# Kernel optimization log

Measured on AMD Instinct MI355X. Metric: run time of the kernel, lower is better.

## Reference

```python
import jax, jax.numpy as jnp
import numpy as np

NUM_BASE = 92
NUM_NOVEL = 40
GAMMA = 2.0
ALPHA = 0.25
DISTIL_FACTOR = 1.0
BSZ, N_DET, DIM_FEAT, DIM_HID, DIM_EMB = 16, 48, 2048, 1024, 512
EMB_HALF = DIM_EMB // 2


def _pair_ids(n):
    # all ordered pairs (i, j), i != j  (trajid2pairid)
    s, o = np.meshgrid(np.arange(n), np.arange(n), indexing='ij')
    m = s != o
    return s[m].astype(np.int32), o[m].astype(np.int32)


def _norm(x, eps=1e-12):
    # F.normalize(dim=-1)
    return x / jnp.maximum(jnp.linalg.norm(x, axis=-1, keepdims=True), eps)


def _sigmoid_focal_loss(logits, targets):
    # torchvision.ops.sigmoid_focal_loss, alpha=0.25, gamma=2, reduction='none'
    p = jax.nn.sigmoid(logits)
    ce = jnp.maximum(logits, 0) - logits * targets + jnp.log1p(jnp.exp(-jnp.abs(logits)))
    p_t = p * targets + (1.0 - p) * (1.0 - targets)
    loss = ce * (1.0 - p_t) ** GAMMA
    a_t = ALPHA * targets + (1.0 - ALPHA) * (1.0 - targets)
    return a_t * loss


def setup_inputs() -> dict:
    key = jax.random.key(0)
    ks = jax.random.split(key, 12)
    sids_np, oids_np = _pair_ids(N_DET)
    P = sids_np.shape[0]  # 2256 pairs per video
    w = lambda k, shape, s=0.02: jax.random.normal(k, shape, dtype=jnp.float32) * s
    return {
        'det_feats': jax.random.normal(ks[0], (BSZ, N_DET, DIM_FEAT), dtype=jnp.float32),
        'traj_embds': jax.random.normal(ks[1], (BSZ, N_DET, EMB_HALF), dtype=jnp.float32),
        'relpos_feats': jax.random.normal(ks[2], (BSZ, P, 12), dtype=jnp.float32),
        'classifier_weights': _norm(jax.random.normal(ks[3], (NUM_BASE, DIM_EMB), dtype=jnp.float32)) / np.sqrt(2.0),
        'W1': w(ks[4], (2 * DIM_FEAT, DIM_HID)), 'b1': jnp.zeros((DIM_HID,), jnp.float32),
        'W2': w(ks[5], (DIM_HID, DIM_HID)), 'b2': jnp.zeros((DIM_HID,), jnp.float32),
        'W3': w(ks[6], (DIM_HID, DIM_EMB)),
        'R1': w(ks[7], (12, 256), 0.1), 'rb1': jnp.zeros((256,), jnp.float32),
        'R2': w(ks[8], (256, DIM_EMB), 0.1),
        'temperature': jnp.full((1,), 0.02, dtype=jnp.float32),
        'labels': jax.random.randint(ks[9], (BSZ, P, 1 + NUM_BASE + NUM_NOVEL), 0, 2, dtype=jnp.int32),
        'sids': jnp.asarray(sids_np),
        'oids': jnp.asarray(oids_np),
    }


def reference(det_feats, traj_embds, relpos_feats, classifier_weights,
              W1, b1, W2, b2, W3, R1, rb1, R2, temperature,
              labels, sids, oids):
    Df = det_feats.shape[-1]
    De = traj_embds.shape[-1]
    # gather subject / object features for all pairs, flatten batch
    s_f = det_feats[:, sids, :].reshape(-1, Df)   # [N, Df]
    o_f = det_feats[:, oids, :].reshape(-1, Df)
    so = jnp.concatenate([s_f, o_f], axis=-1)      # [N, 2*Df]
    # trajpair_proj MLP
    h = jax.nn.relu(so @ W1 + b1)
    h = jax.nn.relu(h @ W2 + b2)
    so_proj = h @ W3                                # [N, dim_emb]
    so_n = _norm(so_proj)
    # relpos branch
    rp = relpos_feats.reshape(-1, relpos_feats.shape[-1])
    re = jax.nn.relu(rp @ R1 + rb1) @ R2
    re = _norm(re)
    combined = _norm(so_n + re)
    logits = (combined @ classifier_weights.T) / temperature  # [N, num_base]
    # cls_loss_on_base
    lab = labels.reshape(-1, 1 + NUM_BASE + NUM_NOVEL).astype(logits.dtype)
    pos_mask = jnp.any(lab[:, 1:1 + NUM_BASE] > 0, axis=-1)
    neg_mask = lab[:, 0] > 0
    lab_base = lab[:, 1:1 + NUM_BASE]
    fl_pos = _sigmoid_focal_loss(logits, lab_base)
    pos_den = jnp.maximum(pos_mask.sum(), 1).astype(logits.dtype) * NUM_BASE
    pos_loss = jnp.sum(fl_pos * pos_mask[:, None]) / pos_den
    fl_neg = _sigmoid_focal_loss(logits, jnp.zeros_like(logits))
    neg_den = jnp.maximum(neg_mask.sum(), 1).astype(logits.dtype) * NUM_BASE
    neg_loss = jnp.sum(fl_neg * neg_mask[:, None]) / neg_den
    # distillation L1 loss
    s_e = traj_embds[:, sids, :].reshape(-1, De)
    o_e = traj_embds[:, oids, :].reshape(-1, De)
    distil_target = jnp.concatenate([s_e, o_e], axis=-1)  # [N, dim_emb]
    distil_loss = jnp.mean(jnp.abs(distil_target - so_proj)) * DISTIL_FACTOR
    total_loss = pos_loss + neg_loss + distil_loss
    return total_loss
```

## Files before the change

### kernel.cpp

```cpp
#include <hip/hip_runtime.h>
#include <math.h>

constexpr int BSZ   = 16;
constexpr int NDET  = 48;
constexpr int PAIRS = NDET * (NDET - 1);
constexpr int ROWS  = BSZ * PAIRS;
constexpr int DF    = 2048;
constexpr int DH    = 1024;
constexpr int DE    = 512;
constexpr int EHALF = 256;
constexpr int NCLS  = 92;
constexpr int NPAD  = 128;
constexpr int LABW  = 1 + 92 + 40;

typedef __attribute__((ext_vector_type(8))) short bf16x8;
typedef __attribute__((ext_vector_type(4))) float f32x4;

__device__ __forceinline__ short f2bf(float f) {
    union { float f; unsigned u; } a; a.f = f;
    unsigned r = a.u + 0x7fffu + ((a.u >> 16) & 1u);
    return (short)(r >> 16);
}
__device__ __forceinline__ float bf2f(short h) {
    union { unsigned u; float f; } x;
    x.u = ((unsigned)(unsigned short)h) << 16;
    return x.f;
}

constexpr int N4DET = BSZ * NDET * DF / 4;
constexpr int N4CWT = NPAD * DE / 4;
constexpr int NCONVB = (N4DET + N4CWT) / 256;

struct TransJobs {
    const float* src[5];
    short*       dst[5];
    int K[5], N[5];
    int cum[6];
};

__global__ __launch_bounds__(256) void prep_kernel(
    const float* __restrict__ det, short* __restrict__ det_bf,
    const float* __restrict__ cw, short* __restrict__ cwt, TransJobs jobs)
{
    if (blockIdx.x < NCONVB) {
        int i = blockIdx.x * 256 + threadIdx.x;
        if (i < N4DET) {
            float4 v = ((const float4*)det)[i];
            short4 o;
            o.x = f2bf(v.x); o.y = f2bf(v.y); o.z = f2bf(v.z); o.w = f2bf(v.w);
            ((short4*)det_bf)[i] = o;
        } else {
            int k = i - N4DET;
            int n = (k * 4) >> 9;
            short4 o = {0, 0, 0, 0};
            if (n < NCLS) {
                float4 v = ((const float4*)cw)[k];
                o.x = f2bf(v.x); o.y = f2bf(v.y); o.z = f2bf(v.z); o.w = f2bf(v.w);
            }
            ((short4*)cwt)[k] = o;
        }
        return;
    }
    __shared__ float tile[32][33];
    int t = blockIdx.x - NCONVB;
    int j = 0;
    while (t >= jobs.cum[j + 1]) ++j;
    int lt = t - jobs.cum[j];
    int K = jobs.K[j], N = jobs.N[j];
    int nx = N >> 5;
    int ky = lt / nx, nxi = lt - ky * nx;
    int n0 = nxi * 32, k0 = ky * 32;
    const float* src = jobs.src[j];
    short* dst = jobs.dst[j];
    int tx = threadIdx.x & 31, ty = threadIdx.x >> 5;
#pragma unroll
    for (int i = ty; i < 32; i += 8)
        tile[i][tx] = src[(size_t)(k0 + i) * N + n0 + tx];
    __syncthreads();
#pragma unroll
    for (int i = ty; i < 32; i += 8)
        dst[(size_t)(n0 + i) * K + k0 + tx] = f2bf(tile[tx][i]);
}

__device__ __forceinline__ void load16_lds(const void* g, void* l) {
    __builtin_amdgcn_global_load_lds(
        (const __attribute__((address_space(1))) unsigned int*)g,
        (__attribute__((address_space(3))) unsigned int*)l, 16, 0, 0);
}

template <bool BIAS, bool RELU, bool OUTBF16, bool SWIZZLE, bool DUAL>
__global__ __launch_bounds__(256, 4) void mfma_gemm(
    const short* __restrict__ A, const short* __restrict__ Bt,
    const float* __restrict__ bias, void* __restrict__ C,
    int M, int N, int K, int lda, int ldb,
    const short* A2, const short* Bt2, void* C2, int nsplit,
    int K2, int lda2, int ldb2)
{
    __shared__ __align__(16) char smem_raw[17408];
    short* As = (short*)smem_raw;
    short* Bs = As + 128 * 32;

    int bx, by;
    if (SWIZZLE) {
        int nb  = gridDim.x;
        int gid = blockIdx.y * nb + blockIdx.x;
        int xcd = gid & 7;
        int j   = gid >> 3;
        int rows_per = gridDim.y >> 3;
        int lr  = j / nb;
        bx = j - lr * nb;
        by = xcd * rows_per + lr;
    } else {
        bx = blockIdx.x; by = blockIdx.y;
    }
    if (DUAL && bx >= nsplit) {
        bx -= nsplit; A = A2; Bt = Bt2; C = C2; K = K2; lda = lda2; ldb = ldb2;
    }
    if (by * 128 >= M) return;

    const int tid  = threadIdx.x;
    const int wave = tid >> 6;
    const int lane = tid & 63;
    const int m0 = by * 128;
    const int n0 = bx * 128;
    const int wm = (wave & 1) * 64;
    const int wn = (wave >> 1) * 64;

    f32x4 acc[4][4] = {};

    const int q  = lane >> 4;
    const int lm = lane & 15;

    for (int k0 = 0; k0 < K; k0 += 32) {
#pragma unroll
        for (int it = 0; it < 2; ++it) {
            int c   = it * 256 + tid;
            int row = c >> 2;
            int kk  = (c & 3) * 8;
            int ldsc = (it * 256 + wave * 64) * 8;
            int gm = m0 + row; if (gm >= M) gm = M - 1;
            load16_lds(A + (size_t)gm * lda + k0 + kk, As + ldsc);
            int gn = n0 + row;
            load16_lds(Bt + (size_t)gn * ldb + k0 + kk, Bs + ldsc);
        }
        __syncthreads();

        bf16x8 af[4], bfr[4];
#pragma unroll
        for (int t = 0; t < 4; ++t) {
            af[t]  = *(const bf16x8*)(As + (wm + t * 16 + lm) * 32 + q * 8);
            bfr[t] = *(const bf16x8*)(Bs + (wn + t * 16 + lm) * 32 + q * 8);
        }
#pragma unroll
        for (int tm = 0; tm < 4; ++tm)
#pragma unroll
            for (int tn = 0; tn < 4; ++tn)
                acc[tm][tn] = __builtin_amdgcn_mfma_f32_16x16x32_bf16(
                    af[tm], bfr[tn], acc[tm][tn], 0, 0, 0);
        __syncthreads();
    }

    if (OUTBF16) {
        float* scratch = (float*)smem_raw + wave * (16 * 68);
#pragma unroll
        for (int tm = 0; tm < 4; ++tm) {
            __syncthreads();
#pragma unroll
            for (int tn = 0; tn < 4; ++tn) {
                float bv = BIAS ? bias[n0 + wn + tn * 16 + lm] : 0.0f;
#pragma unroll
                for (int r = 0; r < 4; ++r) {
                    float v = acc[tm][tn][r] + bv;
                    if (RELU) v = fmaxf(v, 0.0f);
                    scratch[(q * 4 + r) * 68 + tn * 16 + lm] = v;
                }
            }
            __syncthreads();
#pragma unroll
            for (int p = 0; p < 2; ++p) {
                int row16 = (lane >> 3) + p * 8;
                int c0 = (lane & 7) * 8;
                float4 v0 = *(float4*)&scratch[row16 * 68 + c0];
                float4 v1 = *(float4*)&scratch[row16 * 68 + c0 + 4];
                bf16x8 o;
                o[0] = f2bf(v0.x); o[1] = f2bf(v0.y); o[2] = f2bf(v0.z); o[3] = f2bf(v0.w);
                o[4] = f2bf(v1.x); o[5] = f2bf(v1.y); o[6] = f2bf(v1.z); o[7] = f2bf(v1.w);
                int grow = m0 + wm + tm * 16 + row16;
                if (grow < M)
                    *(bf16x8*)((short*)C + (size_t)grow * N + n0 + wn + c0) = o;
            }
        }
    } else {
#pragma unroll
        for (int tm = 0; tm < 4; ++tm)
#pragma unroll
            for (int tn = 0; tn < 4; ++tn) {
                int col = n0 + wn + tn * 16 + lm;
#pragma unroll
                for (int r = 0; r < 4; ++r) {
                    int row = m0 + wm + tm * 16 + q * 4 + r;
                    if (row < M) {
                        float v = acc[tm][tn][r];
                        if (BIAS) v += bias[col];
                        if (RELU) v = fmaxf(v, 0.0f);
                        ((float*)C)[(size_t)row * N + col] = v;
                    }
                }
            }
    }
}

__global__ __launch_bounds__(256) void pairs_rh_kernel(
    const short* __restrict__ UVa, const short* __restrict__ UVb,
    const float* __restrict__ b1,
    const int* __restrict__ sids, const int* __restrict__ oids,
    short* __restrict__ h1,
    const float* __restrict__ rp, const float* __restrict__ R1,
    const float* __restrict__ rb1, short* __restrict__ rh, int b0)
{
    int r = blockIdx.x;
    int b = b0 + r / PAIRS;
    int p = r % PAIRS;
    int j = threadIdx.x;

    size_t soff = (size_t)(b * NDET + sids[p]) * 2048;
    size_t ooff = (size_t)(b * NDET + oids[p]) * 2048 + 1024;
    short4 a1 = ((const short4*)(UVa + soff))[j];
    short4 a2 = ((const short4*)(UVb + soff))[j];
    short4 a3 = ((const short4*)(UVa + ooff))[j];
    short4 a4 = ((const short4*)(UVb + ooff))[j];
    float4 bb = ((const float4*)b1)[j];
    short4 h;
    h.x = f2bf(fmaxf(bf2f(a1.x) + bf2f(a2.x) + bf2f(a3.x) + bf2f(a4.x) + bb.x, 0.0f));
    h.y = f2bf(fmaxf(bf2f(a1.y) + bf2f(a2.y) + bf2f(a3.y) + bf2f(a4.y) + bb.y, 0.0f));
    h.z = f2bf(fmaxf(bf2f(a1.z) + bf2f(a2.z) + bf2f(a3.z) + bf2f(a4.z) + bb.z, 0.0f));
    h.w = f2bf(fmaxf(bf2f(a1.w) + bf2f(a2.w) + bf2f(a3.w) + bf2f(a4.w) + bb.w, 0.0f));
    ((short4*)(h1 + (size_t)r * DH))[j] = h;

    int rg = b0 * PAIRS + r;
    const float* row = rp + (size_t)rg * 12;
    float acc = rb1[j];
#pragma unroll
    for (int k = 0; k < 12; ++k) acc = fmaf(row[k], R1[k * 256 + j], acc);
    rh[(size_t)r * 256 + j] = f2bf(fmaxf(acc, 0.0f));
}

__global__ __launch_bounds__(256) void row_prep_kernel(
    const short* __restrict__ sp_bf, const short* __restrict__ ru_bf,
    const float* __restrict__ traj, const float* __restrict__ temperature,
    const int* __restrict__ sids, const int* __restrict__ oids,
    short* __restrict__ comb_bf, float* __restrict__ dist_arr, int b0)
{
    int wave = threadIdx.x >> 6, lane = threadIdx.x & 63;
    int r = blockIdx.x * 4 + wave;
    int rg = b0 * PAIRS + r;
    int b = b0 + r / PAIRS;
    int p = r % PAIRS;

    bf16x8 sv = ((const bf16x8*)(sp_bf + (size_t)r * DE))[lane];
    bf16x8 uv = ((const bf16x8*)(ru_bf + (size_t)r * DE))[lane];
    float s[8], u[8];
#pragma unroll
    for (int i = 0; i < 8; ++i) { s[i] = bf2f(sv[i]); u[i] = bf2f(uv[i]); }

    const float* tsrc = (lane < 32)
        ? (traj + (size_t)(b * NDET + sids[p]) * EHALF + lane * 8)
        : (traj + (size_t)(b * NDET + oids[p]) * EHALF + (lane - 32) * 8);
    float4 t0 = ((const float4*)tsrc)[0], t1 = ((const float4*)tsrc)[1];
    float t[8] = {t0.x, t0.y, t0.z, t0.w, t1.x, t1.y, t1.z, t1.w};

    float ss = 0.0f, sr = 0.0f, sd = 0.0f;
#pragma unroll
    for (int i = 0; i < 8; ++i) {
        ss += s[i] * s[i];
        sr += u[i] * u[i];
        sd += fabsf(t[i] - s[i]);
    }
#pragma unroll
    for (int m = 1; m < 64; m <<= 1) {
        ss += __shfl_xor(ss, m);
        sr += __shfl_xor(sr, m);
        sd += __shfl_xor(sd, m);
    }
    float inv_s = 1.0f / fmaxf(sqrtf(ss), 1e-12f);
    float inv_r = 1.0f / fmaxf(sqrtf(sr), 1e-12f);

    float c[8], sc = 0.0f;
#pragma unroll
    for (int i = 0; i < 8; ++i) {
        c[i] = s[i] * inv_s + u[i] * inv_r;
        sc += c[i] * c[i];
    }
#pragma unroll
    for (int m = 1; m < 64; m <<= 1) sc += __shfl_xor(sc, m);

    float scale = (1.0f / fmaxf(sqrtf(sc), 1e-12f)) / temperature[0];

    bf16x8 o;
#pragma unroll
    for (int i = 0; i < 8; ++i) o[i] = f2bf(c[i] * scale);
    ((bf16x8*)(comb_bf + (size_t)r * DE))[lane] = o;

    if (lane == 0) dist_arr[rg] = sd;
}

__global__ __launch_bounds__(256) void focal_kernel(
    const float* __restrict__ logits, const int* __restrict__ labels,
    float4* __restrict__ pn, int b0)
{
    int wave = threadIdx.x >> 6, lane = threadIdx.x & 63;
    int r = blockIdx.x * 4 + wave;
    int rg = b0 * PAIRS + r;
    const float* lrow = logits + (size_t)r * NPAD;
    size_t labbase = (size_t)rg * LABW;

    float flp = 0.0f, fln = 0.0f, fm = 0.0f;
    for (int c = lane; c < NCLS; c += 64) {
        float l = lrow[c];
        int t = labels[labbase + 1 + c];
        if (t > 0) fm = 1.0f;
        float tf = (float)t;
        float pr = 1.0f / (1.0f + expf(-l));
        float lg = log1pf(expf(-fabsf(l)));
        float ce = fmaxf(l, 0.0f) - l * tf + lg;
        float pt = pr * tf + (1.0f - pr) * (1.0f - tf);
        float om = 1.0f - pt;
        float at = 0.25f * tf + 0.75f * (1.0f - tf);
        flp += at * ce * om * om;
        float ce0 = fmaxf(l, 0.0f) + lg;
        fln += 0.75f * ce0 * pr * pr;
    }
#pragma unroll
    for (int m = 1; m < 64; m <<= 1) {
        flp += __shfl_xor(flp, m);
        fln += __shfl_xor(fln, m);
        fm  += __shfl_xor(fm, m);
    }
    if (lane == 0) {
        int posf = (fm > 0.5f) ? 1 : 0;
        int negf = (labels[labbase] > 0) ? 1 : 0;
        pn[rg] = make_float4(posf ? flp : 0.0f, negf ? fln : 0.0f, 0.0f,
                             (float)(posf + 2 * negf));
    }
}

struct RedRec { double sp, sn, sd; int cp, cn; };
constexpr int RED1 = 64;
constexpr int ROWS_PER_RED = ROWS / RED1;

__global__ __launch_bounds__(256) void reduce1_kernel(
    const float4* __restrict__ pn, const float* __restrict__ dist_arr,
    RedRec* __restrict__ scratch)
{
    int tid = threadIdx.x;
    int base = blockIdx.x * ROWS_PER_RED;
    double sp = 0.0, sn = 0.0, sd = 0.0;
    int cp = 0, cn = 0;
    for (int i = tid; i < ROWS_PER_RED; i += 256) {
        float4 v = pn[base + i];
        sp += (double)v.x; sn += (double)v.y; sd += (double)dist_arr[base + i];
        int f = (int)v.w;
        cp += f & 1; cn += (f >> 1) & 1;
    }
    __shared__ double A[256], B[256], C[256];
    __shared__ int I[256], J[256];
    A[tid] = sp; B[tid] = sn; C[tid] = sd; I[tid] = cp; J[tid] = cn;
    __syncthreads();
    for (int st = 128; st > 0; st >>= 1) {
        if (tid < st) { A[tid] += A[tid + st]; B[tid] += B[tid + st]; C[tid] += C[tid + st];
                        I[tid] += I[tid + st]; J[tid] += J[tid + st]; }
        __syncthreads();
    }
    if (tid == 0) {
        RedRec rec; rec.sp = A[0]; rec.sn = B[0]; rec.sd = C[0];
        rec.cp = I[0]; rec.cn = J[0];
        scratch[blockIdx.x] = rec;
    }
}

__global__ __launch_bounds__(64) void reduce2_kernel(
    const RedRec* __restrict__ scratch, float* __restrict__ out)
{
    int lane = threadIdx.x;
    RedRec rec = scratch[lane];
    double sp = rec.sp, sn = rec.sn, sd = rec.sd;
    int cp = rec.cp, cn = rec.cn;
#pragma unroll
    for (int m = 1; m < 64; m <<= 1) {
        sp += __shfl_xor(sp, m);
        sn += __shfl_xor(sn, m);
        sd += __shfl_xor(sd, m);
        cp += __shfl_xor(cp, m);
        cn += __shfl_xor(cn, m);
    }
    if (lane == 0) {
        int cpv = cp < 1 ? 1 : cp;
        int cnv = cn < 1 ? 1 : cn;
        out[0] = (float)(sp / ((double)cpv * NCLS) +
                         sn / ((double)cnv * NCLS) +
                         sd / ((double)ROWS * DE));
    }
}

static inline int pad8(int x) { return (x + 7) & ~7; }

extern "C" void kernel_launch(void* const* d_in, const int* in_sizes, int n_in,
                              void* d_out, int out_size, void* d_ws, size_t ws_size,
                              hipStream_t stream)
{
    const float* det    = (const float*)d_in[0];
    const float* traj   = (const float*)d_in[1];
    const float* relpos = (const float*)d_in[2];
    const float* cw     = (const float*)d_in[3];
    const float* W1     = (const float*)d_in[4];
    const float* b1     = (const float*)d_in[5];
    const float* W2     = (const float*)d_in[6];
    const float* b2     = (const float*)d_in[7];
    const float* W3     = (const float*)d_in[8];
    const float* R1     = (const float*)d_in[9];
    const float* rb1    = (const float*)d_in[10];
    const float* R2     = (const float*)d_in[11];
    const float* temp   = (const float*)d_in[12];
    const int*   labels = (const int*)d_in[13];
    const int*   sids   = (const int*)d_in[14];
    const int*   oids   = (const int*)d_in[15];
    float* out = (float*)d_out;

    char* ws = (char*)d_ws;
    size_t off = 0;
    auto carve = [&](size_t bytes) -> char* {
        char* p = ws + off;
        off = (off + bytes + 255) & ~(size_t)255;
        return p;
    };
    float4* pn       = (float4*)carve((size_t)ROWS * 16);
    float*  dist_arr = (float*)carve((size_t)ROWS * 4);
    short*  det_bf   = (short*)carve((size_t)BSZ * NDET * DF * 2);
    short*  W1t      = (short*)carve((size_t)2048 * 2048 * 2);
    short*  W2t      = (short*)carve((size_t)DH * DH * 2);
    short*  W3t      = (short*)carve((size_t)DE * DH * 2);
    short*  R2t      = (short*)carve((size_t)DE * 256 * 2);
    short*  cwt      = (short*)carve((size_t)NPAD * DE * 2);
    short*  UVa      = (short*)carve((size_t)BSZ * NDET * 2048 * 2);
    short*  UVb      = (short*)carve((size_t)BSZ * NDET * 2048 * 2);
    size_t fixed_off = off;

    int b_ch = 1;
    for (int cand : {16, 8, 4, 2, 1}) {
        size_t rows  = (size_t)cand * PAIRS;
        size_t bytes = fixed_off + rows * 2048 + 256 + rows * 2048 + 256
                     + rows * 512 + 256 + rows * 1024 + 256;
        if (bytes <= ws_size) { b_ch = cand; break; }
    }
    const int chunk_rows = b_ch * PAIRS;
    const int n_chunks = BSZ / b_ch;
    char* reg1 = carve((size_t)chunk_rows * 2048);
    char* reg2 = carve((size_t)chunk_rows * 2048);
    char* reg3 = carve((size_t)chunk_rows * 512);
    short* comb_bf = (short*)carve((size_t)chunk_rows * 1024);

    short* h1      = (short*)reg1;
    short* h2      = (short*)reg2;
    short* so_bf   = (short*)reg1;
    short* re_bf   = (short*)reg2;
    short* rh      = (short*)reg3;
    float* logits  = (float*)reg3;
    RedRec* red_scratch = (RedRec*)comb_bf;

    TransJobs tj;
    tj.src[0] = W1;                    tj.dst[0] = W1t;                   tj.K[0] = DF;  tj.N[0] = DH;
    tj.src[1] = W1 + (size_t)DF * DH;  tj.dst[1] = W1t + (size_t)DH * DF; tj.K[1] = DF;  tj.N[1] = DH;
    tj.src[2] = W2;                    tj.dst[2] = W2t;                   tj.K[2] = DH;  tj.N[2] = DH;
    tj.src[3] = W3;                    tj.dst[3] = W3t;                   tj.K[3] = DH;  tj.N[3] = DE;
    tj.src[4] = R2;                    tj.dst[4] = R2t;                   tj.K[4] = 256; tj.N[4] = DE;
    tj.cum[0] = 0;
    for (int i = 0; i < 5; ++i)
        tj.cum[i + 1] = tj.cum[i] + (tj.K[i] / 32) * (tj.N[i] / 32);
    prep_kernel<<<NCONVB + tj.cum[5], 256, 0, stream>>>(det, det_bf, cw, cwt, tj);

    mfma_gemm<false, false, true, false, true>
        <<<dim3(32, 6), 256, 0, stream>>>(
        det_bf, W1t, nullptr, UVa, BSZ * NDET, 2048, 1024, 2048, 2048,
        det_bf + 1024, W1t + 1024, UVb, 16, 1024, 2048, 2048);

    const int mg  = (chunk_rows + 127) / 128;
    const int mgp = pad8(mg);

    for (int c = 0; c < n_chunks; ++c) {
        int b0 = c * b_ch;
        int r0 = b0 * PAIRS;

        pairs_rh_kernel<<<chunk_rows, 256, 0, stream>>>(
            UVa, UVb, b1, sids, oids, h1, relpos, R1, rb1, rh, b0);

        mfma_gemm<true, true, true, true, false>
            <<<dim3(DH / 128, mgp), 256, 0, stream>>>(
            h1, W2t, b2, h2, chunk_rows, DH, DH, DH, DH,
            nullptr, nullptr, nullptr, 0, 0, 0, 0);

        mfma_gemm<false, false, true, true, true>
            <<<dim3(8, mgp), 256, 0, stream>>>(
            h2, W3t, nullptr, so_bf, chunk_rows, DE, DH, DH, DH,
            rh, R2t, re_bf, 4, 256, 256, 256);

        row_prep_kernel<<<chunk_rows / 4, 256, 0, stream>>>(
            so_bf, re_bf, traj, temp, sids, oids, comb_bf, dist_arr, b0);

        mfma_gemm<false, false, false, true, false>
            <<<dim3(1, mgp), 256, 0, stream>>>(
            comb_bf, cwt, nullptr, logits, chunk_rows, NPAD, DE, DE, DE,
            nullptr, nullptr, nullptr, 0, 0, 0, 0);

        focal_kernel<<<chunk_rows / 4, 256, 0, stream>>>(logits, labels, pn, b0);
    }

    reduce1_kernel<<<RED1, 256, 0, stream>>>(pn, dist_arr, red_scratch);
    reduce2_kernel<<<1, 64, 0, stream>>>(red_scratch, out);
}
```

Measured before the change: 423.3 us.

## Double GEMM K-step to 64 and premerge UV halves before pair gather

The MFMA GEMM now stages 64 K-elements per iteration, in two 32-wide halves in LDS, so each tile needs half as many loop iterations and barrier pairs. LDS use grows from about 17KB to 32KB, which may limit occupancy under launch_bounds(256,4). A new uvmerge kernel adds the two K-split partial results UVa and UVb once, plus bias on the subject half, so the per-pair gather reads two vectors instead of four and drops the bias load. This trades an extra small kernel launch for much less gather traffic. The merged sum is rounded to bf16 before the pair addition, which slightly changes rounding.

```diff
diff --git a/kernel.cpp b/kernel.cpp
--- a/kernel.cpp
+++ b/kernel.cpp
@@ -96,9 +96,9 @@
     const short* A2, const short* Bt2, void* C2, int nsplit,
     int K2, int lda2, int ldb2)
 {
-    __shared__ __align__(16) char smem_raw[17408];
+    __shared__ __align__(16) char smem_raw[32768];
     short* As = (short*)smem_raw;
-    short* Bs = As + 128 * 32;
+    short* Bs = As + 128 * 64;
 
     int bx, by;
     if (SWIZZLE) {
@@ -131,13 +131,14 @@
     const int q  = lane >> 4;
     const int lm = lane & 15;
 
-    for (int k0 = 0; k0 < K; k0 += 32) {
-#pragma unroll
-        for (int it = 0; it < 2; ++it) {
-            int c   = it * 256 + tid;
-            int row = c >> 2;
-            int kk  = (c & 3) * 8;
-            int ldsc = (it * 256 + wave * 64) * 8;
+    for (int k0 = 0; k0 < K; k0 += 64) {
+#pragma unroll
+        for (int it = 0; it < 4; ++it) {
+            int c    = (it & 1) * 256 + tid;
+            int half = it >> 1;
+            int row  = c >> 2;
+            int kk   = (c & 3) * 8 + half * 32;
+            int ldsc = half * 4096 + ((it & 1) * 256 + wave * 64) * 8;
             int gm = m0 + row; if (gm >= M) gm = M - 1;
             load16_lds(A + (size_t)gm * lda + k0 + kk, As + ldsc);
             int gn = n0 + row;
@@ -145,18 +146,23 @@
         }
         __syncthreads();
 
-        bf16x8 af[4], bfr[4];
-#pragma unroll
-        for (int t = 0; t < 4; ++t) {
-            af[t]  = *(const bf16x8*)(As + (wm + t * 16 + lm) * 32 + q * 8);
-            bfr[t] = *(const bf16x8*)(Bs + (wn + t * 16 + lm) * 32 + q * 8);
+#pragma unroll
+        for (int half = 0; half < 2; ++half) {
+            const short* Ah = As + half * 4096;
+            const short* Bh = Bs + half * 4096;
+            bf16x8 af[4], bfr[4];
+#pragma unroll
+            for (int t = 0; t < 4; ++t) {
+                af[t]  = *(const bf16x8*)(Ah + (wm + t * 16 + lm) * 32 + q * 8);
+                bfr[t] = *(const bf16x8*)(Bh + (wn + t * 16 + lm) * 32 + q * 8);
+            }
+#pragma unroll
+            for (int tm = 0; tm < 4; ++tm)
+#pragma unroll
+                for (int tn = 0; tn < 4; ++tn)
+                    acc[tm][tn] = __builtin_amdgcn_mfma_f32_16x16x32_bf16(
+                        af[tm], bfr[tn], acc[tm][tn], 0, 0, 0);
         }
-#pragma unroll
-        for (int tm = 0; tm < 4; ++tm)
-#pragma unroll
-            for (int tn = 0; tn < 4; ++tn)
-                acc[tm][tn] = __builtin_amdgcn_mfma_f32_16x16x32_bf16(
-                    af[tm], bfr[tn], acc[tm][tn], 0, 0, 0);
         __syncthreads();
     }
 
@@ -210,9 +216,28 @@
     }
 }
 
+constexpr int N4UV = BSZ * NDET * 2048 / 4;
+__global__ __launch_bounds__(256) void uvmerge_kernel(
+    short* __restrict__ UVa, const short* __restrict__ UVb,
+    const float* __restrict__ b1)
+{
+    int i = blockIdx.x * 256 + threadIdx.x;
+    if (i >= N4UV) return;
+    short4 a = ((const short4*)UVa)[i];
+    short4 b = ((const short4*)UVb)[i];
+    int col4 = i & 511;
+    float4 bb = {0.0f, 0.0f, 0.0f, 0.0f};
+    if (col4 < 256) bb = ((const float4*)b1)[col4];
+    short4 o;
+    o.x = f2bf(bf2f(a.x) + bf2f(b.x) + bb.x);
+    o.y = f2bf(bf2f(a.y) + bf2f(b.y) + bb.y);
+    o.z = f2bf(bf2f(a.z) + bf2f(b.z) + bb.z);
+    o.w = f2bf(bf2f(a.w) + bf2f(b.w) + bb.w);
+    ((short4*)UVa)[i] = o;
+}
+
 __global__ __launch_bounds__(256) void pairs_rh_kernel(
-    const short* __restrict__ UVa, const short* __restrict__ UVb,
-    const float* __restrict__ b1,
+    const short* __restrict__ UVs,
     const int* __restrict__ sids, const int* __restrict__ oids,
     short* __restrict__ h1,
     const float* __restrict__ rp, const float* __restrict__ R1,
@@ -225,16 +250,13 @@
 
     size_t soff = (size_t)(b * NDET + sids[p]) * 2048;
     size_t ooff = (size_t)(b * NDET + oids[p]) * 2048 + 1024;
-    short4 a1 = ((const short4*)(UVa + soff))[j];
-    short4 a2 = ((const short4*)(UVb + soff))[j];
-    short4 a3 = ((const short4*)(UVa + ooff))[j];
-    short4 a4 = ((const short4*)(UVb + ooff))[j];
-    float4 bb = ((const float4*)b1)[j];
+    short4 a1 = ((const short4*)(UVs + soff))[j];
+    short4 a3 = ((const short4*)(UVs + ooff))[j];
     short4 h;
-    h.x = f2bf(fmaxf(bf2f(a1.x) + bf2f(a2.x) + bf2f(a3.x) + bf2f(a4.x) + bb.x, 0.0f));
-    h.y = f2bf(fmaxf(bf2f(a1.y) + bf2f(a2.y) + bf2f(a3.y) + bf2f(a4.y) + bb.y, 0.0f));
-    h.z = f2bf(fmaxf(bf2f(a1.z) + bf2f(a2.z) + bf2f(a3.z) + bf2f(a4.z) + bb.z, 0.0f));
-    h.w = f2bf(fmaxf(bf2f(a1.w) + bf2f(a2.w) + bf2f(a3.w) + bf2f(a4.w) + bb.w, 0.0f));
+    h.x = f2bf(fmaxf(bf2f(a1.x) + bf2f(a3.x), 0.0f));
+    h.y = f2bf(fmaxf(bf2f(a1.y) + bf2f(a3.y), 0.0f));
+    h.z = f2bf(fmaxf(bf2f(a1.z) + bf2f(a3.z), 0.0f));
+    h.w = f2bf(fmaxf(bf2f(a1.w) + bf2f(a3.w), 0.0f));
     ((short4*)(h1 + (size_t)r * DH))[j] = h;
 
     int rg = b0 * PAIRS + r;
@@ -483,6 +505,8 @@
         det_bf, W1t, nullptr, UVa, BSZ * NDET, 2048, 1024, 2048, 2048,
         det_bf + 1024, W1t + 1024, UVb, 16, 1024, 2048, 2048);
 
+    uvmerge_kernel<<<(N4UV + 255) / 256, 256, 0, stream>>>(UVa, UVb, b1);
+
     const int mg  = (chunk_rows + 127) / 128;
     const int mgp = pad8(mg);
 
@@ -491,7 +515,7 @@
         int r0 = b0 * PAIRS;
 
         pairs_rh_kernel<<<chunk_rows, 256, 0, stream>>>(
-            UVa, UVb, b1, sids, oids, h1, relpos, R1, rb1, rh, b0);
+            UVa, sids, oids, h1, relpos, R1, rb1, rh, b0);
 
         mfma_gemm<true, true, true, true, false>
             <<<dim3(DH / 128, mgp), 256, 0, stream>>>(
```

Measured after the change: 393.7 us. 7.0% less time.
